# Kernel tuning notes

Hardware: AMD Instinct MI355X
Metric: run time of the kernel (lower is better)

The kernel has to match this reference:

```python
import jax, jax.numpy as jnp
import numpy as np
from jax import lax

B, S, W = 128, 256, 20
WV, CV = 50000, 100
WE, CE, CC, HID = 300, 50, 100, 512
T = 12
START, STOP, PAD = 9, 10, 11
NEG = -10000.0
H = HID // 2           # per-direction hidden
DIN = WE + CC          # LSTM input dim


def setup_inputs() -> dict:
    key = jax.random.key(0)
    ks = jax.random.split(key, 20)
    word_idxs = jax.random.randint(ks[0], (B, S), 0, WV)
    char_idxs = jax.random.randint(ks[1], (B, S, W), 0, CV)
    lengths = jax.random.randint(ks[2], (B,), S // 2, S + 1)
    mask = (jnp.arange(S)[None, :] < lengths[:, None]).astype(jnp.int32)  # prefix valid mask
    word_table = jax.random.normal(ks[3], (WV, WE), jnp.float32)
    char_table = jax.random.normal(ks[4], (CV, CE), jnp.float32)
    conv_w = jax.random.normal(ks[5], (CC, CE, 3), jnp.float32) / np.sqrt(CE * 3)
    conv_b = jnp.zeros((CC,), jnp.float32)
    sc = 1.0 / np.sqrt(H)
    u = lambda k, shp: jax.random.uniform(k, shp, jnp.float32, -sc, sc)
    w_ih_f = u(ks[6], (4 * H, DIN)); w_hh_f = u(ks[7], (4 * H, H))
    b_ih_f = u(ks[8], (4 * H,));    b_hh_f = u(ks[9], (4 * H,))
    w_ih_b = u(ks[10], (4 * H, DIN)); w_hh_b = u(ks[11], (4 * H, H))
    b_ih_b = u(ks[12], (4 * H,));   b_hh_b = u(ks[13], (4 * H,))
    h2t_w = u(ks[14], (T, HID)); h2t_b = u(ks[15], (T,))
    transitions = jax.random.normal(ks[16], (T, T), jnp.float32)
    transitions = transitions.at[START, :].set(NEG).at[:, STOP].set(NEG)
    transitions = transitions.at[PAD, :].set(NEG).at[:, PAD].set(NEG)
    return dict(word_idxs=word_idxs, char_idxs=char_idxs, mask=mask,
                word_table=word_table, char_table=char_table,
                conv_w=conv_w, conv_b=conv_b,
                w_ih_f=w_ih_f, w_hh_f=w_hh_f, b_ih_f=b_ih_f, b_hh_f=b_hh_f,
                w_ih_b=w_ih_b, w_hh_b=w_hh_b, b_ih_b=b_ih_b, b_hh_b=b_hh_b,
                h2t_w=h2t_w, h2t_b=h2t_b, transitions=transitions)


def _lstm_dir(xs, w_ih, w_hh, b, reverse):
    # xs: (S, B, DIN); torch gate order i, f, g, o
    def step(carry, x_t):
        h, c = carry
        g = x_t @ w_ih.T + h @ w_hh.T + b
        i, f, gg, o = jnp.split(g, 4, axis=-1)
        c = jax.nn.sigmoid(f) * c + jax.nn.sigmoid(i) * jnp.tanh(gg)
        h = jax.nn.sigmoid(o) * jnp.tanh(c)
        return (h, c), h
    z = jnp.zeros((xs.shape[1], w_hh.shape[1]), xs.dtype)
    _, hs = lax.scan(step, (z, z), xs, reverse=reverse)
    return hs  # (S, B, H)


def _features(word_idxs, char_idxs, word_table, char_table, conv_w, conv_b,
              w_ih_f, w_hh_f, b_ih_f, b_hh_f, w_ih_b, w_hh_b, b_ih_b, b_hh_b,
              h2t_w, h2t_b):
    we = word_table[word_idxs]                       # (B,S,WE)
    ce = char_table[char_idxs]                       # (B,S,W,CE)
    x = ce.reshape(B * S, W, CE).transpose(0, 2, 1)  # (BS,CE,W)
    conv = lax.conv_general_dilated(x, conv_w, (1,), [(1, 1)],
                                    dimension_numbers=('NCH', 'OIH', 'NCH'))
    conv = jax.nn.relu(conv + conv_b[None, :, None])
    cfeat = conv.max(axis=2).reshape(B, S, CC)       # char max-pool
    emb = jnp.concatenate([we, cfeat], axis=-1)      # (B,S,DIN)
    xs = emb.transpose(1, 0, 2)                      # (S,B,DIN)
    h_f = _lstm_dir(xs, w_ih_f, w_hh_f, b_ih_f + b_hh_f, False)
    h_b = _lstm_dir(xs, w_ih_b, w_hh_b, b_ih_b + b_hh_b, True)
    lstm_out = jnp.concatenate([h_f, h_b], axis=-1).transpose(1, 0, 2)  # (B,S,HID)
    return lstm_out @ h2t_w.T + h2t_b                # (B,S,T)


def reference(word_idxs, char_idxs, mask, word_table, char_table, conv_w, conv_b,
              w_ih_f, w_hh_f, b_ih_f, b_hh_f, w_ih_b, w_hh_b, b_ih_b, b_hh_b,
              h2t_w, h2t_b, transitions):
    feats = _features(word_idxs, char_idxs, word_table, char_table, conv_w, conv_b,
                      w_ih_f, w_hh_f, b_ih_f, b_hh_f, w_ih_b, w_hh_b, b_ih_b, b_hh_b,
                      h2t_w, h2t_b)
    # ---- batched Viterbi ----
    alpha0 = jnp.full((B, T), NEG, feats.dtype).at[:, START].set(0.0)
    def vstep(alpha, inp):
        feat_i, valid = inp                                   # (B,T), (B,)
        scores = alpha[:, :, None] + transitions[None] + feat_i[:, None, :]  # (B,prev,next)
        bp = jnp.argmax(scores, axis=1)                       # (B,T)
        new_alpha = scores.max(axis=1)
        alpha = jnp.where(valid[:, None] > 0, new_alpha, alpha)
        return alpha, bp
    alpha, bps = lax.scan(vstep, alpha0, (feats.transpose(1, 0, 2), mask.T))
    alpha = alpha + transitions[STOP][None, :]
    best_scores = alpha.max(axis=1)
    best_last = jnp.argmax(alpha, axis=1)                     # (B,)
    # ---- vectorized backtrace (skips padded tail, fills PAD) ----
    lengths = mask.sum(axis=1)
    def btstep(tag, inp):
        bp_i, i = inp
        valid = i < lengths                                   # (B,)
        out = jnp.where(valid, tag, PAD)
        prev = jnp.take_along_axis(bp_i, tag[:, None], axis=1)[:, 0]
        tag = jnp.where(valid, prev, tag)
        return tag, out
    _, path = lax.scan(btstep, best_last, (bps, jnp.arange(S)), reverse=True)
    best_paths = path.T                                       # (B,S)
    return best_scores, best_paths
```

## Files before the change

### kernel.cpp

```cpp
#include <hip/hip_runtime.h>

#define BB 128
#define SS 256
#define WW 20
#define WE 300
#define CE 50
#define CC 100
#define DIN 400
#define HID 512
#define Hh 256
#define TT 12
#define START_TAG 9
#define STOP_TAG 10
#define PAD_TAG 11
#define NEGV (-10000.0f)
#define BS 32768
#define CH 32
#define NCH 8
#define CR 4096

#define FULL_NEEDED_BYTES 96731136ull

__global__ __launch_bounds__(256) void k_embedF(
    const int* __restrict__ widx, const int* __restrict__ cidx,
    const float* __restrict__ wtab, const float* __restrict__ ctab,
    const float* __restrict__ convw, const float* __restrict__ convb,
    float* __restrict__ emb)
{
    __shared__ __align__(16) float ce_sh[2][CE][24];
    __shared__ int cid_sh[2][WW];
    __shared__ int wid_sh[2];
    const int tid = threadIdx.x;
    const int pl0 = blockIdx.x * 2;

    int g[2];
    #pragma unroll
    for (int p = 0; p < 2; p++) {
        int pl = pl0 + p;
        int s = pl >> 7, b = pl & 127;
        g[p] = b * SS + s;
    }

    if (tid < 2 * WW) {
        int p = tid / WW, w = tid % WW;
        cid_sh[p][w] = cidx[g[p] * WW + w];
    }
    if (tid < 2) wid_sh[tid] = widx[g[tid]];
    for (int i = tid; i < 2 * CE * 24; i += 256) ((float*)ce_sh)[i] = 0.f;
    __syncthreads();

    for (int i = tid; i < 2 * WW * CE; i += 256) {
        int p = i / (WW * CE);
        int rem = i % (WW * CE);
        int w = rem / CE, ce = rem % CE;
        ce_sh[p][ce][w + 1] = ctab[cid_sh[p][w] * CE + ce];
    }
    for (int i = tid; i < 2 * WE; i += 256) {
        int p = i / WE, col = i % WE;
        emb[(size_t)(pl0 + p) * DIN + col] = wtab[(size_t)wid_sh[p] * WE + col];
    }
    __syncthreads();

    const int p = tid >> 7;
    const int cc = tid & 127;
    if (cc < CC) {
        float acc[WW];
        #pragma unroll
        for (int w = 0; w < WW; w++) acc[w] = 0.f;
        for (int ce = 0; ce < CE; ce++) {
            float row[24];
            #pragma unroll
            for (int q = 0; q < 6; q++) {
                float4 v = *(const float4*)&ce_sh[p][ce][q * 4];
                row[q * 4 + 0] = v.x; row[q * 4 + 1] = v.y;
                row[q * 4 + 2] = v.z; row[q * 4 + 3] = v.w;
            }
            float c0 = convw[(cc * CE + ce) * 3 + 0];
            float c1 = convw[(cc * CE + ce) * 3 + 1];
            float c2 = convw[(cc * CE + ce) * 3 + 2];
            #pragma unroll
            for (int w = 0; w < WW; w++)
                acc[w] += c0 * row[w] + c1 * row[w + 1] + c2 * row[w + 2];
        }
        float bb = convb[cc];
        float m = 0.f;
        #pragma unroll
        for (int w = 0; w < WW; w++) {
            float v = acc[w] + bb;
            v = v > 0.f ? v : 0.f;
            m = v > m ? v : m;
        }
        emb[(size_t)(pl0 + p) * DIN + WE + cc] = m;
    }
}

__global__ __launch_bounds__(256) void k_embedC(
    const int* __restrict__ widx, const int* __restrict__ cidx,
    const float* __restrict__ wtab, const float* __restrict__ ctab,
    const float* __restrict__ convw, const float* __restrict__ convb,
    float* __restrict__ embC, int c)
{
    __shared__ __align__(16) float ce_sh[2][CE][24];
    __shared__ int cid_sh[2][WW];
    __shared__ int wid_sh[2];
    const int tid = threadIdx.x;
    const int pl0 = blockIdx.x * 2;

    int part[2], lr[2], g[2];
    #pragma unroll
    for (int p = 0; p < 2; p++) {
        int pl = pl0 + p;
        part[p] = pl >> 12;
        lr[p] = pl & 4095;
        int ls = lr[p] >> 7;
        int b = lr[p] & 127;
        int s = part[p] ? (224 - 32 * c + ls) : (32 * c + ls);
        g[p] = b * SS + s;
    }

    if (tid < 2 * WW) {
        int p = tid / WW, w = tid % WW;
        cid_sh[p][w] = cidx[g[p] * WW + w];
    }
    if (tid < 2) wid_sh[tid] = widx[g[tid]];
    for (int i = tid; i < 2 * CE * 24; i += 256) ((float*)ce_sh)[i] = 0.f;
    __syncthreads();

    for (int i = tid; i < 2 * WW * CE; i += 256) {
        int p = i / (WW * CE);
        int rem = i % (WW * CE);
        int w = rem / CE, ce = rem % CE;
        ce_sh[p][ce][w + 1] = ctab[cid_sh[p][w] * CE + ce];
    }
    for (int i = tid; i < 2 * WE; i += 256) {
        int p = i / WE, col = i % WE;
        embC[(size_t)(part[p] * CR + lr[p]) * DIN + col] =
            wtab[(size_t)wid_sh[p] * WE + col];
    }
    __syncthreads();

    const int p = tid >> 7;
    const int cc = tid & 127;
    if (cc < CC) {
        float acc[WW];
        #pragma unroll
        for (int w = 0; w < WW; w++) acc[w] = 0.f;
        for (int ce = 0; ce < CE; ce++) {
            float row[24];
            #pragma unroll
            for (int q = 0; q < 6; q++) {
                float4 v = *(const float4*)&ce_sh[p][ce][q * 4];
                row[q * 4 + 0] = v.x; row[q * 4 + 1] = v.y;
                row[q * 4 + 2] = v.z; row[q * 4 + 3] = v.w;
            }
            float c0 = convw[(cc * CE + ce) * 3 + 0];
            float c1 = convw[(cc * CE + ce) * 3 + 1];
            float c2 = convw[(cc * CE + ce) * 3 + 2];
            #pragma unroll
            for (int w = 0; w < WW; w++)
                acc[w] += c0 * row[w] + c1 * row[w + 1] + c2 * row[w + 2];
        }
        float bb = convb[cc];
        float m = 0.f;
        #pragma unroll
        for (int w = 0; w < WW; w++) {
            float v = acc[w] + bb;
            v = v > 0.f ? v : 0.f;
            m = v > m ? v : m;
        }
        embC[(size_t)(part[p] * CR + lr[p]) * DIN + WE + cc] = m;
    }
}

__global__ __launch_bounds__(256) void k_projC(
    const float* __restrict__ ef, const float* __restrict__ eb,
    const float* __restrict__ wih_f, const float* __restrict__ wih_b,
    const float* __restrict__ bih_f, const float* __restrict__ bhh_f,
    const float* __restrict__ bih_b, const float* __restrict__ bhh_b,
    float* __restrict__ gatesC)
{
    __shared__ __align__(16) float As[8][132];
    __shared__ __align__(16) float Bs[8][132];
    const int tid = threadIdx.x;
    const int rt = blockIdx.x;
    const int jt = blockIdx.y;
    const int tx = tid & 15, ty = tid >> 4;
    const int lj = tid >> 1;
    const int kh = (tid & 1) * 4;

    float acc[8][8];
    #pragma unroll
    for (int i = 0; i < 8; i++)
        #pragma unroll
        for (int j = 0; j < 8; j++) acc[i][j] = 0.f;

    const int jg = jt * 128 + lj;
    const float* wsrc = (jg < 1024) ? wih_f : wih_b;
    const int jj = jg & 1023;
    const float* esrc = (jt >= 8) ? eb : ef;

    for (int k0 = 0; k0 < DIN; k0 += 8) {
        float4 av = *(const float4*)&wsrc[(size_t)jj * DIN + k0 + kh];
        float4 bv = *(const float4*)&esrc[(size_t)(rt * 128 + lj) * DIN + k0 + kh];
        __syncthreads();
        As[kh + 0][lj] = av.x; As[kh + 1][lj] = av.y; As[kh + 2][lj] = av.z; As[kh + 3][lj] = av.w;
        Bs[kh + 0][lj] = bv.x; Bs[kh + 1][lj] = bv.y; Bs[kh + 2][lj] = bv.z; Bs[kh + 3][lj] = bv.w;
        __syncthreads();
        #pragma unroll
        for (int kk = 0; kk < 8; kk++) {
            float4 a0 = *(const float4*)&As[kk][ty * 8];
            float4 a1 = *(const float4*)&As[kk][ty * 8 + 4];
            float4 b0 = *(const float4*)&Bs[kk][tx * 8];
            float4 b1 = *(const float4*)&Bs[kk][tx * 8 + 4];
            float aa[8] = {a0.x, a0.y, a0.z, a0.w, a1.x, a1.y, a1.z, a1.w};
            float bbv[8] = {b0.x, b0.y, b0.z, b0.w, b1.x, b1.y, b1.z, b1.w};
            #pragma unroll
            for (int i = 0; i < 8; i++)
                #pragma unroll
                for (int j = 0; j < 8; j++) acc[i][j] += aa[i] * bbv[j];
        }
    }

    #pragma unroll
    for (int i = 0; i < 8; i++) {
        int j = jt * 128 + ty * 8 + i;
        int dir = j >> 10;
        int jr = j & 1023;
        float bias = dir ? (bih_b[jr] + bhh_b[jr]) : (bih_f[jr] + bhh_f[jr]);
        size_t base = (size_t)j * CR + rt * 128 + tx * 8;
        float4 o0 = {acc[i][0] + bias, acc[i][1] + bias, acc[i][2] + bias, acc[i][3] + bias};
        float4 o1 = {acc[i][4] + bias, acc[i][5] + bias, acc[i][6] + bias, acc[i][7] + bias};
        *(float4*)&gatesC[base] = o0;
        *(float4*)&gatesC[base + 4] = o1;
    }
}

__global__ __launch_bounds__(256) void k_step2(
    const float* __restrict__ gatesC,
    const float* __restrict__ whh_f, const float* __restrict__ whh_b,
    float* __restrict__ hbuf, float* __restrict__ cbuf, float* __restrict__ lstmC,
    int t)
{
    __shared__ float psum[4][128];
    const int tid = threadIdx.x;
    const int b = tid & 127;
    const int kh = tid >> 7;
    const int blk = blockIdx.x;
    const int dir = blk >> 8;
    const int kg = blk & 255;
    const int tl = t & (CH - 1);
    const int lr = (dir ? (CH - 1 - tl) : tl) * BB + b;

    float q0 = 0.f, q1 = 0.f, q2 = 0.f, q3 = 0.f, c_old = 0.f;
    const int jb = dir * 1024;
    if (kh == 0) {
        q0 = gatesC[(size_t)(jb + 0 * Hh + kg) * CR + lr];
        q1 = gatesC[(size_t)(jb + 1 * Hh + kg) * CR + lr];
        q2 = gatesC[(size_t)(jb + 2 * Hh + kg) * CR + lr];
        q3 = gatesC[(size_t)(jb + 3 * Hh + kg) * CR + lr];
        if (t > 0) c_old = cbuf[(size_t)(dir * Hh + kg) * BB + b];
    }

    float g0 = 0.f, g1 = 0.f, g2 = 0.f, g3 = 0.f;
    if (t > 0) {
        const float* whh = dir ? whh_b : whh_f;
        const int koff = __builtin_amdgcn_readfirstlane(kh * 128);
        const float* w0 = whh + (size_t)(0 * Hh + kg) * Hh + koff;
        const float* w1 = whh + (size_t)(1 * Hh + kg) * Hh + koff;
        const float* w2 = whh + (size_t)(2 * Hh + kg) * Hh + koff;
        const float* w3 = whh + (size_t)(3 * Hh + kg) * Hh + koff;
        const int par = t & 1;
        const float* hsrc = hbuf + (size_t)((par * 2 + dir) * Hh + koff) * BB;
        #pragma unroll 4
        for (int kk = 0; kk < 128; kk += 4) {
            float h0 = hsrc[(kk + 0) * BB + b];
            float h1 = hsrc[(kk + 1) * BB + b];
            float h2 = hsrc[(kk + 2) * BB + b];
            float h3 = hsrc[(kk + 3) * BB + b];
            float4 wa = *(const float4*)&w0[kk];
            float4 wb = *(const float4*)&w1[kk];
            float4 wc = *(const float4*)&w2[kk];
            float4 wd = *(const float4*)&w3[kk];
            g0 += h0 * wa.x + h1 * wa.y + h2 * wa.z + h3 * wa.w;
            g1 += h0 * wb.x + h1 * wb.y + h2 * wb.z + h3 * wb.w;
            g2 += h0 * wc.x + h1 * wc.y + h2 * wc.z + h3 * wc.w;
            g3 += h0 * wd.x + h1 * wd.y + h2 * wd.z + h3 * wd.w;
        }
    }

    if (kh) {
        psum[0][b] = g0; psum[1][b] = g1; psum[2][b] = g2; psum[3][b] = g3;
    }
    __syncthreads();
    if (!kh) {
        g0 = (q0 + g0) + psum[0][b];
        g1 = (q1 + g1) + psum[1][b];
        g2 = (q2 + g2) + psum[2][b];
        g3 = (q3 + g3) + psum[3][b];

        float si = 1.f / (1.f + expf(-g0));
        float sf = 1.f / (1.f + expf(-g1));
        float tg = tanhf(g2);
        float so = 1.f / (1.f + expf(-g3));
        float c_new = sf * c_old + si * tg;
        float h_new = so * tanhf(c_new);

        cbuf[(size_t)(dir * Hh + kg) * BB + b] = c_new;
        const int parn = (t + 1) & 1;
        hbuf[(size_t)((parn * 2 + dir) * Hh + kg) * BB + b] = h_new;
        lstmC[(size_t)(dir * Hh + kg) * CR + lr] = h_new;
    }
}

__global__ __launch_bounds__(256) void k_feats_init(
    const float* __restrict__ h2b, float* __restrict__ feats)
{
    int i = blockIdx.x * 256 + threadIdx.x;
    if (i < BS * TT) feats[i] = h2b[i % TT];
}

__global__ __launch_bounds__(256) void k_feats_acc(
    const float* __restrict__ lstmC,
    const float* __restrict__ h2w, float* __restrict__ feats, int c)
{
    __shared__ float ps[TT][128];
    const int part = blockIdx.x >> 5;
    const int ls = blockIdx.x & 31;
    const int b = threadIdx.x & 127;
    const int kh = threadIdx.x >> 7;
    const int s = part ? (224 - 32 * c + ls) : (32 * c + ls);
    const int r = s * BB + b;
    const int k0 = kh * 128;

    float acc[TT];
    #pragma unroll
    for (int t = 0; t < TT; t++) acc[t] = 0.f;
    for (int dk = 0; dk < 128; dk++) {
        float v = lstmC[(size_t)(part * Hh + k0 + dk) * CR + ls * BB + b];
        #pragma unroll
        for (int t = 0; t < TT; t++) acc[t] += v * h2w[t * HID + part * Hh + k0 + dk];
    }
    if (kh) {
        #pragma unroll
        for (int t = 0; t < TT; t++) ps[t][b] = acc[t];
    }
    __syncthreads();
    if (!kh) {
        #pragma unroll
        for (int t = 0; t < TT; t++)
            feats[(size_t)r * TT + t] += acc[t] + ps[t][b];
    }
}

__global__ __launch_bounds__(64) void k_viterbi(
    const float* __restrict__ feats,
    const int* __restrict__ mask, const float* __restrict__ trans,
    float* __restrict__ out)
{
    __shared__ unsigned char bp_sh[SS][TT];
    __shared__ int red[64];
    __shared__ int len_sh;
    const int b = blockIdx.x;
    const int tid = threadIdx.x;
    const int n = tid;

    int partial = 0;
    for (int s = tid; s < SS; s += 64) partial += mask[b * SS + s];
    red[tid] = partial;
    __syncthreads();
    if (tid == 0) {
        int L = 0;
        for (int i = 0; i < 64; i++) L += red[i];
        len_sh = L;
    }
    __syncthreads();
    const int len = len_sh;

    float tr[TT];
    float alpha = NEGV;
    if (n < TT) {
        #pragma unroll
        for (int p = 0; p < TT; p++) tr[p] = trans[p * TT + n];
        alpha = (n == START_TAG) ? 0.f : NEGV;
    }

    for (int s = 0; s < len; s++) {
        float feat = (n < TT) ? feats[(size_t)(s * BB + b) * TT + n] : 0.f;
        float best = -3.0e38f;
        int bpi = 0;
        #pragma unroll
        for (int p = 0; p < TT; p++) {
            float ap = __shfl(alpha, p, 64);
            float sc = (n < TT) ? ((ap + tr[p]) + feat) : -3.0e38f;
            if (sc > best) { best = sc; bpi = p; }
        }
        if (n < TT) {
            bp_sh[s][n] = (unsigned char)bpi;
            alpha = best;
        }
    }

    float term = (n < TT) ? (alpha + trans[STOP_TAG * TT + n]) : -3.0e38f;
    float bs = -3.0e38f;
    int bl = 0;
    #pragma unroll
    for (int p = 0; p < TT; p++) {
        float v = __shfl(term, p, 64);
        if (v > bs) { bs = v; bl = p; }
    }

    if (tid == 0) {
        out[b] = bs;
        int tag = bl;
        for (int s = SS - 1; s >= 0; s--) {
            float o;
            if (s < len) {
                o = (float)tag;
                tag = (int)bp_sh[s][tag];
            } else {
                o = (float)PAD_TAG;
            }
            out[BB + b * SS + s] = o;
        }
    }
}

extern "C" void kernel_launch(void* const* d_in, const int* in_sizes, int n_in,
                              void* d_out, int out_size, void* d_ws, size_t ws_size,
                              hipStream_t stream) {
    const int*   widx  = (const int*)d_in[0];
    const int*   cidx  = (const int*)d_in[1];
    const int*   mask  = (const int*)d_in[2];
    const float* wtab  = (const float*)d_in[3];
    const float* ctab  = (const float*)d_in[4];
    const float* convw = (const float*)d_in[5];
    const float* convb = (const float*)d_in[6];
    const float* wih_f = (const float*)d_in[7];
    const float* whh_f = (const float*)d_in[8];
    const float* bih_f = (const float*)d_in[9];
    const float* bhh_f = (const float*)d_in[10];
    const float* wih_b = (const float*)d_in[11];
    const float* whh_b = (const float*)d_in[12];
    const float* bih_b = (const float*)d_in[13];
    const float* bhh_b = (const float*)d_in[14];
    const float* h2w   = (const float*)d_in[15];
    const float* h2b   = (const float*)d_in[16];
    const float* trans = (const float*)d_in[17];

    const bool full = ws_size >= FULL_NEEDED_BYTES;
    float* ws = (float*)d_ws;
    float* emb    = ws;
    const size_t emb_fl = full ? (size_t)BS * DIN : (size_t)2 * CR * DIN;
    float* gatesC = emb + emb_fl;
    float* lstmC  = gatesC + (size_t)2048 * CR;
    float* feats  = lstmC + (size_t)HID * CR;
    float* hbuf   = feats + (size_t)BS * TT;
    float* cbuf   = hbuf + (size_t)4 * Hh * BB;

    hipLaunchKernelGGL(k_feats_init, dim3((BS * TT + 255) / 256), dim3(256), 0, stream,
                       h2b, feats);
    if (full) {
        hipLaunchKernelGGL(k_embedF, dim3(BS / 2), dim3(256), 0, stream,
                           widx, cidx, wtab, ctab, convw, convb, emb);
    }
    for (int c = 0; c < NCH; c++) {
        if (!full) {
            hipLaunchKernelGGL(k_embedC, dim3(CR), dim3(256), 0, stream,
                               widx, cidx, wtab, ctab, convw, convb, emb, c);
        }
        const float* ef = full ? (emb + (size_t)(32 * c * BB) * DIN) : emb;
        const float* eb = full ? (emb + (size_t)((224 - 32 * c) * BB) * DIN)
                               : (emb + (size_t)CR * DIN);
        hipLaunchKernelGGL(k_projC, dim3(CR / 128, 16), dim3(256), 0, stream,
                           ef, eb, wih_f, wih_b, bih_f, bhh_f, bih_b, bhh_b, gatesC);
        for (int tl = 0; tl < CH; tl++) {
            hipLaunchKernelGGL(k_step2, dim3(512), dim3(256), 0, stream,
                               gatesC, whh_f, whh_b, hbuf, cbuf, lstmC, c * CH + tl);
        }
        hipLaunchKernelGGL(k_feats_acc, dim3(64), dim3(256), 0, stream,
                           lstmC, h2w, feats, c);
    }
    hipLaunchKernelGGL(k_viterbi, dim3(BB), dim3(64), 0, stream, feats, mask, trans, (float*)d_out);
}
```

Measured before the change: 3.417 ms.

## Restructure LSTM recurrent step into per-thread full-K dot products with batch-major hidden state

The recurrent step kernel now gives each thread one (batch, hidden-unit) pair and loops over the whole 256-wide hidden input, instead of splitting K across two half-blocks joined by a shared-memory reduction. The hidden-state buffer is switched to batch-major so each thread can read its row with float4 loads. The grid is halved to 256 blocks, and the syncthreads and idle half-block in the epilogue are gone. The cost is a serial loop twice as long per thread, strided rather than coalesced h loads across lanes, and weight loads that are no longer wave-uniform.

```diff
diff --git a/kernel.cpp b/kernel.cpp
--- a/kernel.cpp
+++ b/kernel.cpp
@@ -235,81 +235,64 @@
     }
 }
 
-__global__ __launch_bounds__(256) void k_step2(
+__global__ __launch_bounds__(256) void k_step3(
     const float* __restrict__ gatesC,
     const float* __restrict__ whh_f, const float* __restrict__ whh_b,
     float* __restrict__ hbuf, float* __restrict__ cbuf, float* __restrict__ lstmC,
     int t)
 {
-    __shared__ float psum[4][128];
     const int tid = threadIdx.x;
-    const int b = tid & 127;
-    const int kh = tid >> 7;
+    const int bb = tid & 31;
+    const int ko = tid >> 5;
     const int blk = blockIdx.x;
-    const int dir = blk >> 8;
-    const int kg = blk & 255;
+    const int dir = blk >> 7;
+    const int kot = (blk >> 2) & 31;
+    const int bq  = blk & 3;
+    const int b   = bq * 32 + bb;
+    const int kout = kot * 8 + ko;
     const int tl = t & (CH - 1);
-    const int lr = (dir ? (CH - 1 - tl) : tl) * BB + b;
-
-    float q0 = 0.f, q1 = 0.f, q2 = 0.f, q3 = 0.f, c_old = 0.f;
-    const int jb = dir * 1024;
-    if (kh == 0) {
-        q0 = gatesC[(size_t)(jb + 0 * Hh + kg) * CR + lr];
-        q1 = gatesC[(size_t)(jb + 1 * Hh + kg) * CR + lr];
-        q2 = gatesC[(size_t)(jb + 2 * Hh + kg) * CR + lr];
-        q3 = gatesC[(size_t)(jb + 3 * Hh + kg) * CR + lr];
-        if (t > 0) c_old = cbuf[(size_t)(dir * Hh + kg) * BB + b];
-    }
-
-    float g0 = 0.f, g1 = 0.f, g2 = 0.f, g3 = 0.f;
+    const int ls = dir ? (CH - 1 - tl) : tl;
+    const int lr = ls * BB + b;
+    const int jb = dir * 4 * Hh;
+
+    float g0 = gatesC[(size_t)(jb + 0 * Hh + kout) * CR + lr];
+    float g1 = gatesC[(size_t)(jb + 1 * Hh + kout) * CR + lr];
+    float g2 = gatesC[(size_t)(jb + 2 * Hh + kout) * CR + lr];
+    float g3 = gatesC[(size_t)(jb + 3 * Hh + kout) * CR + lr];
+    float c_old = 0.f;
+    if (t > 0) c_old = cbuf[(dir * Hh + kout) * BB + b];
+
     if (t > 0) {
         const float* whh = dir ? whh_b : whh_f;
-        const int koff = __builtin_amdgcn_readfirstlane(kh * 128);
-        const float* w0 = whh + (size_t)(0 * Hh + kg) * Hh + koff;
-        const float* w1 = whh + (size_t)(1 * Hh + kg) * Hh + koff;
-        const float* w2 = whh + (size_t)(2 * Hh + kg) * Hh + koff;
-        const float* w3 = whh + (size_t)(3 * Hh + kg) * Hh + koff;
-        const int par = t & 1;
-        const float* hsrc = hbuf + (size_t)((par * 2 + dir) * Hh + koff) * BB;
+        const float* w0 = whh + (size_t)(0 * Hh + kout) * Hh;
+        const float* w1 = whh + (size_t)(1 * Hh + kout) * Hh;
+        const float* w2 = whh + (size_t)(2 * Hh + kout) * Hh;
+        const float* w3 = whh + (size_t)(3 * Hh + kout) * Hh;
+        const float* hrow = hbuf + (size_t)(((t & 1) * 2 + dir) * BB + b) * Hh;
         #pragma unroll 4
-        for (int kk = 0; kk < 128; kk += 4) {
-            float h0 = hsrc[(kk + 0) * BB + b];
-            float h1 = hsrc[(kk + 1) * BB + b];
-            float h2 = hsrc[(kk + 2) * BB + b];
-            float h3 = hsrc[(kk + 3) * BB + b];
-            float4 wa = *(const float4*)&w0[kk];
-            float4 wb = *(const float4*)&w1[kk];
-            float4 wc = *(const float4*)&w2[kk];
-            float4 wd = *(const float4*)&w3[kk];
-            g0 += h0 * wa.x + h1 * wa.y + h2 * wa.z + h3 * wa.w;
-            g1 += h0 * wb.x + h1 * wb.y + h2 * wb.z + h3 * wb.w;
-            g2 += h0 * wc.x + h1 * wc.y + h2 * wc.z + h3 * wc.w;
-            g3 += h0 * wd.x + h1 * wd.y + h2 * wd.z + h3 * wd.w;
-        }
-    }
-
-    if (kh) {
-        psum[0][b] = g0; psum[1][b] = g1; psum[2][b] = g2; psum[3][b] = g3;
-    }
-    __syncthreads();
-    if (!kh) {
-        g0 = (q0 + g0) + psum[0][b];
-        g1 = (q1 + g1) + psum[1][b];
-        g2 = (q2 + g2) + psum[2][b];
-        g3 = (q3 + g3) + psum[3][b];
-
-        float si = 1.f / (1.f + expf(-g0));
-        float sf = 1.f / (1.f + expf(-g1));
-        float tg = tanhf(g2);
-        float so = 1.f / (1.f + expf(-g3));
-        float c_new = sf * c_old + si * tg;
-        float h_new = so * tanhf(c_new);
-
-        cbuf[(size_t)(dir * Hh + kg) * BB + b] = c_new;
-        const int parn = (t + 1) & 1;
-        hbuf[(size_t)((parn * 2 + dir) * Hh + kg) * BB + b] = h_new;
-        lstmC[(size_t)(dir * Hh + kg) * CR + lr] = h_new;
-    }
+        for (int kin = 0; kin < Hh; kin += 4) {
+            float4 hv = *(const float4*)&hrow[kin];
+            float4 wa = *(const float4*)&w0[kin];
+            float4 wb = *(const float4*)&w1[kin];
+            float4 wc = *(const float4*)&w2[kin];
+            float4 wd = *(const float4*)&w3[kin];
+            g0 += hv.x * wa.x + hv.y * wa.y + hv.z * wa.z + hv.w * wa.w;
+            g1 += hv.x * wb.x + hv.y * wb.y + hv.z * wb.z + hv.w * wb.w;
+            g2 += hv.x * wc.x + hv.y * wc.y + hv.z * wc.z + hv.w * wc.w;
+            g3 += hv.x * wd.x + hv.y * wd.y + hv.z * wd.z + hv.w * wd.w;
+        }
+    }
+
+    float si = 1.f / (1.f + expf(-g0));
+    float sf = 1.f / (1.f + expf(-g1));
+    float tg = tanhf(g2);
+    float so = 1.f / (1.f + expf(-g3));
+    float c_new = sf * c_old + si * tg;
+    float h_new = so * tanhf(c_new);
+
+    cbuf[(dir * Hh + kout) * BB + b] = c_new;
+    hbuf[(size_t)((((t + 1) & 1) * 2 + dir) * BB + b) * Hh + kout] = h_new;
+    lstmC[(size_t)(dir * Hh + kout) * CR + lr] = h_new;
 }
 
 __global__ __launch_bounds__(256) void k_feats_init(
@@ -474,7 +457,7 @@
         hipLaunchKernelGGL(k_projC, dim3(CR / 128, 16), dim3(256), 0, stream,
                            ef, eb, wih_f, wih_b, bih_f, bhh_f, bih_b, bhh_b, gatesC);
         for (int tl = 0; tl < CH; tl++) {
-            hipLaunchKernelGGL(k_step2, dim3(512), dim3(256), 0, stream,
+            hipLaunchKernelGGL(k_step3, dim3(256), dim3(256), 0, stream,
                                gatesC, whh_f, whh_b, hbuf, cbuf, lstmC, c * CH + tl);
         }
         hipLaunchKernelGGL(k_feats_acc, dim3(64), dim3(256), 0, stream,
```

Measured after the change: 6.610 ms. +93.4%, slower.

## Use bf16 MFMA for LSTM input projection with bf16 embeddings and weights

Applied to the files above, without the earlier changes.

Replaces the fp32 SIMT GEMM for the per-chunk input projection with a bf16 MFMA (16x16x32) kernel. Embeddings are now written as bf16 with K padded to 416, and a new pre-pass converts W_ih to bf16 and precomputes the fused biases. The aim is to cut the compute and bandwidth cost of the projection GEMM, at the price of bf16 rounding on the inputs, which could affect accuracy. The workspace layout is reorganized around byte-size constants.

```diff
diff --git a/kernel.cpp b/kernel.cpp
--- a/kernel.cpp
+++ b/kernel.cpp
@@ -7,6 +7,7 @@
 #define CE 50
 #define CC 100
 #define DIN 400
+#define KP 416
 #define HID 512
 #define Hh 256
 #define TT 12
@@ -19,13 +20,51 @@
 #define NCH 8
 #define CR 4096
 
-#define FULL_NEEDED_BYTES 96731136ull
+typedef __attribute__((ext_vector_type(8))) short short8;
+typedef __attribute__((ext_vector_type(4))) float floatx4;
+
+#define SZ_EMB_FULL  27262976ull
+#define SZ_EMB_CHUNK  6815744ull
+#define SZ_WB         1703936ull
+#define SZ_BIAS          8192ull
+#define SZ_GATES     33554432ull
+#define SZ_LSTM       8388608ull
+#define SZ_FEATS      1572864ull
+#define SZ_HBUF        524288ull
+#define SZ_CBUF        262144ull
+#define FULL_NEEDED_BYTES (SZ_EMB_FULL + SZ_WB + SZ_BIAS + SZ_GATES + SZ_LSTM + SZ_FEATS + SZ_HBUF + SZ_CBUF)
+
+__device__ __forceinline__ unsigned short f2bf(float x) {
+    unsigned int u = __builtin_bit_cast(unsigned int, x);
+    unsigned int r = (u + 0x7FFFu + ((u >> 16) & 1u)) >> 16;
+    return (unsigned short)r;
+}
+
+__global__ __launch_bounds__(256) void k_w2b(
+    const float* __restrict__ wih_f, const float* __restrict__ wih_b,
+    const float* __restrict__ bih_f, const float* __restrict__ bhh_f,
+    const float* __restrict__ bih_b, const float* __restrict__ bhh_b,
+    unsigned short* __restrict__ wB, float* __restrict__ biasC)
+{
+    int idx = blockIdx.x * 256 + threadIdx.x;
+    if (idx < 2048 * KP) {
+        int j = idx / KP;
+        int col = idx - j * KP;
+        const float* src = (j < 1024) ? wih_f : wih_b;
+        int jr = j & 1023;
+        wB[idx] = (col < DIN) ? f2bf(src[jr * DIN + col]) : 0;
+    }
+    if (idx < 2048) {
+        int jr = idx & 1023;
+        biasC[idx] = (idx < 1024) ? (bih_f[jr] + bhh_f[jr]) : (bih_b[jr] + bhh_b[jr]);
+    }
+}
 
 __global__ __launch_bounds__(256) void k_embedF(
     const int* __restrict__ widx, const int* __restrict__ cidx,
     const float* __restrict__ wtab, const float* __restrict__ ctab,
     const float* __restrict__ convw, const float* __restrict__ convb,
-    float* __restrict__ emb)
+    unsigned short* __restrict__ embB)
 {
     __shared__ __align__(16) float ce_sh[2][CE][24];
     __shared__ int cid_sh[2][WW];
@@ -57,7 +96,11 @@
     }
     for (int i = tid; i < 2 * WE; i += 256) {
         int p = i / WE, col = i % WE;
-        emb[(size_t)(pl0 + p) * DIN + col] = wtab[(size_t)wid_sh[p] * WE + col];
+        embB[(size_t)(pl0 + p) * KP + col] = f2bf(wtab[(size_t)wid_sh[p] * WE + col]);
+    }
+    for (int i = tid; i < 2 * (KP - DIN); i += 256) {
+        int p = i / (KP - DIN), col = DIN + i % (KP - DIN);
+        embB[(size_t)(pl0 + p) * KP + col] = 0;
     }
     __syncthreads();
 
@@ -90,7 +133,7 @@
             v = v > 0.f ? v : 0.f;
             m = v > m ? v : m;
         }
-        emb[(size_t)(pl0 + p) * DIN + WE + cc] = m;
+        embB[(size_t)(pl0 + p) * KP + WE + cc] = f2bf(m);
     }
 }
 
@@ -98,7 +141,7 @@
     const int* __restrict__ widx, const int* __restrict__ cidx,
     const float* __restrict__ wtab, const float* __restrict__ ctab,
     const float* __restrict__ convw, const float* __restrict__ convb,
-    float* __restrict__ embC, int c)
+    unsigned short* __restrict__ embB, int c)
 {
     __shared__ __align__(16) float ce_sh[2][CE][24];
     __shared__ int cid_sh[2][WW];
@@ -134,8 +177,12 @@
     }
     for (int i = tid; i < 2 * WE; i += 256) {
         int p = i / WE, col = i % WE;
-        embC[(size_t)(part[p] * CR + lr[p]) * DIN + col] =
-            wtab[(size_t)wid_sh[p] * WE + col];
+        embB[(size_t)(part[p] * CR + lr[p]) * KP + col] =
+            f2bf(wtab[(size_t)wid_sh[p] * WE + col]);
+    }
+    for (int i = tid; i < 2 * (KP - DIN); i += 256) {
+        int p = i / (KP - DIN), col = DIN + i % (KP - DIN);
+        embB[(size_t)(part[p] * CR + lr[p]) * KP + col] = 0;
     }
     __syncthreads();
 
@@ -168,70 +215,82 @@
             v = v > 0.f ? v : 0.f;
             m = v > m ? v : m;
         }
-        embC[(size_t)(part[p] * CR + lr[p]) * DIN + WE + cc] = m;
-    }
-}
-
-__global__ __launch_bounds__(256) void k_projC(
-    const float* __restrict__ ef, const float* __restrict__ eb,
-    const float* __restrict__ wih_f, const float* __restrict__ wih_b,
-    const float* __restrict__ bih_f, const float* __restrict__ bhh_f,
-    const float* __restrict__ bih_b, const float* __restrict__ bhh_b,
+        embB[(size_t)(part[p] * CR + lr[p]) * KP + WE + cc] = f2bf(m);
+    }
+}
+
+__global__ __launch_bounds__(256) void k_projB(
+    const unsigned short* __restrict__ ef, const unsigned short* __restrict__ eb,
+    const unsigned short* __restrict__ wB, const float* __restrict__ biasC,
     float* __restrict__ gatesC)
 {
-    __shared__ __align__(16) float As[8][132];
-    __shared__ __align__(16) float Bs[8][132];
+    __shared__ __align__(16) unsigned short Wt[128 * 40];
+    __shared__ __align__(16) unsigned short Et[128 * 40];
     const int tid = threadIdx.x;
     const int rt = blockIdx.x;
     const int jt = blockIdx.y;
-    const int tx = tid & 15, ty = tid >> 4;
-    const int lj = tid >> 1;
-    const int kh = (tid & 1) * 4;
-
-    float acc[8][8];
-    #pragma unroll
-    for (int i = 0; i < 8; i++)
-        #pragma unroll
-        for (int j = 0; j < 8; j++) acc[i][j] = 0.f;
-
-    const int jg = jt * 128 + lj;
-    const float* wsrc = (jg < 1024) ? wih_f : wih_b;
-    const int jj = jg & 1023;
-    const float* esrc = (jt >= 8) ? eb : ef;
-
-    for (int k0 = 0; k0 < DIN; k0 += 8) {
-        float4 av = *(const float4*)&wsrc[(size_t)jj * DIN + k0 + kh];
-        float4 bv = *(const float4*)&esrc[(size_t)(rt * 128 + lj) * DIN + k0 + kh];
+    const unsigned short* esrc = (jt >= 8) ? eb : ef;
+
+    const int row = tid >> 1;
+    const int half = tid & 1;
+    const int lane = tid & 63;
+    const int wv = tid >> 6;
+    const int wm = wv >> 1, wn = wv & 1;
+    const int fr = lane & 15, quad = lane >> 4;
+
+    floatx4 acc[4][4];
+    #pragma unroll
+    for (int i = 0; i < 4; i++)
+        #pragma unroll
+        for (int j = 0; j < 4; j++) acc[i][j] = (floatx4){0.f, 0.f, 0.f, 0.f};
+
+    const unsigned short* wrow = wB + (size_t)(jt * 128 + row) * KP + half * 16;
+    const unsigned short* erow = esrc + (size_t)(rt * 128 + row) * KP + half * 16;
+
+    for (int kt = 0; kt < 13; kt++) {
+        int4 wv0 = *(const int4*)(wrow + kt * 32);
+        int4 wv1 = *(const int4*)(wrow + kt * 32 + 8);
+        int4 ev0 = *(const int4*)(erow + kt * 32);
+        int4 ev1 = *(const int4*)(erow + kt * 32 + 8);
         __syncthreads();
-        As[kh + 0][lj] = av.x; As[kh + 1][lj] = av.y; As[kh + 2][lj] = av.z; As[kh + 3][lj] = av.w;
-        Bs[kh + 0][lj] = bv.x; Bs[kh + 1][lj] = bv.y; Bs[kh + 2][lj] = bv.z; Bs[kh + 3][lj] = bv.w;
+        *(int4*)&Wt[row * 40 + half * 16]     = wv0;
+        *(int4*)&Wt[row * 40 + half * 16 + 8] = wv1;
+        *(int4*)&Et[row * 40 + half * 16]     = ev0;
+        *(int4*)&Et[row * 40 + half * 16 + 8] = ev1;
         __syncthreads();
-        #pragma unroll
-        for (int kk = 0; kk < 8; kk++) {
-            float4 a0 = *(const float4*)&As[kk][ty * 8];
-            float4 a1 = *(const float4*)&As[kk][ty * 8 + 4];
-            float4 b0 = *(const float4*)&Bs[kk][tx * 8];
-            float4 b1 = *(const float4*)&Bs[kk][tx * 8 + 4];
-            float aa[8] = {a0.x, a0.y, a0.z, a0.w, a1.x, a1.y, a1.z, a1.w};
-            float bbv[8] = {b0.x, b0.y, b0.z, b0.w, b1.x, b1.y, b1.z, b1.w};
+
+        short8 af[4], bf[4];
+        #pragma unroll
+        for (int fi = 0; fi < 4; fi++)
+            af[fi] = *(const short8*)&Wt[(wm * 64 + fi * 16 + fr) * 40 + quad * 8];
+        #pragma unroll
+        for (int fj = 0; fj < 4; fj++)
+            bf[fj] = *(const short8*)&Et[(wn * 64 + fj * 16 + fr) * 40 + quad * 8];
+        #pragma unroll
+        for (int fi = 0; fi < 4; fi++)
             #pragma unroll
-            for (int i = 0; i < 8; i++)
-                #pragma unroll
-                for (int j = 0; j < 8; j++) acc[i][j] += aa[i] * bbv[j];
-        }
-    }
-
-    #pragma unroll
-    for (int i = 0; i < 8; i++) {
-        int j = jt * 128 + ty * 8 + i;
-        int dir = j >> 10;
-        int jr = j & 1023;
-        float bias = dir ? (bih_b[jr] + bhh_b[jr]) : (bih_f[jr] + bhh_f[jr]);
-        size_t base = (size_t)j * CR + rt * 128 + tx * 8;
-        float4 o0 = {acc[i][0] + bias, acc[i][1] + bias, acc[i][2] + bias, acc[i][3] + bias};
-        float4 o1 = {acc[i][4] + bias, acc[i][5] + bias, acc[i][6] + bias, acc[i][7] + bias};
-        *(float4*)&gatesC[base] = o0;
-        *(float4*)&gatesC[base + 4] = o1;
+            for (int fj = 0; fj < 4; fj++)
+                acc[fi][fj] = __builtin_amdgcn_mfma_f32_16x16x32_bf16(
+                    af[fi], bf[fj], acc[fi][fj], 0, 0, 0);
+    }
+
+    float bias[4][4];
+    #pragma unroll
+    for (int fi = 0; fi < 4; fi++)
+        #pragma unroll
+        for (int reg = 0; reg < 4; reg++)
+            bias[fi][reg] = biasC[jt * 128 + wm * 64 + fi * 16 + quad * 4 + reg];
+
+    #pragma unroll
+    for (int fi = 0; fi < 4; fi++) {
+        #pragma unroll
+        for (int fj = 0; fj < 4; fj++) {
+            int rg = rt * 128 + wn * 64 + fj * 16 + fr;
+            int jg = jt * 128 + wm * 64 + fi * 16 + quad * 4;
+            #pragma unroll
+            for (int reg = 0; reg < 4; reg++)
+                gatesC[(size_t)(jg + reg) * CR + rg] = acc[fi][fj][reg] + bias[fi][reg];
+        }
     }
 }
 
@@ -448,31 +507,35 @@
     const float* trans = (const float*)d_in[17];
 
     const bool full = ws_size >= FULL_NEEDED_BYTES;
-    float* ws = (float*)d_ws;
-    float* emb    = ws;
-    const size_t emb_fl = full ? (size_t)BS * DIN : (size_t)2 * CR * DIN;
-    float* gatesC = emb + emb_fl;
-    float* lstmC  = gatesC + (size_t)2048 * CR;
-    float* feats  = lstmC + (size_t)HID * CR;
-    float* hbuf   = feats + (size_t)BS * TT;
-    float* cbuf   = hbuf + (size_t)4 * Hh * BB;
+    char* base = (char*)d_ws;
+    const size_t emb_sz = full ? SZ_EMB_FULL : SZ_EMB_CHUNK;
+    unsigned short* embB = (unsigned short*)base;
+    unsigned short* wB   = (unsigned short*)(base + emb_sz);
+    float* biasC  = (float*)(base + emb_sz + SZ_WB);
+    float* gatesC = (float*)(base + emb_sz + SZ_WB + SZ_BIAS);
+    float* lstmC  = (float*)(base + emb_sz + SZ_WB + SZ_BIAS + SZ_GATES);
+    float* feats  = (float*)(base + emb_sz + SZ_WB + SZ_BIAS + SZ_GATES + SZ_LSTM);
+    float* hbuf   = (float*)(base + emb_sz + SZ_WB + SZ_BIAS + SZ_GATES + SZ_LSTM + SZ_FEATS);
+    float* cbuf   = (float*)(base + emb_sz + SZ_WB + SZ_BIAS + SZ_GATES + SZ_LSTM + SZ_FEATS + SZ_HBUF);
 
     hipLaunchKernelGGL(k_feats_init, dim3((BS * TT + 255) / 256), dim3(256), 0, stream,
                        h2b, feats);
+    hipLaunchKernelGGL(k_w2b, dim3((2048 * KP + 255) / 256), dim3(256), 0, stream,
+                       wih_f, wih_b, bih_f, bhh_f, bih_b, bhh_b, wB, biasC);
     if (full) {
         hipLaunchKernelGGL(k_embedF, dim3(BS / 2), dim3(256), 0, stream,
-                           widx, cidx, wtab, ctab, convw, convb, emb);
+                           widx, cidx, wtab, ctab, convw, convb, embB);
     }
     for (int c = 0; c < NCH; c++) {
         if (!full) {
             hipLaunchKernelGGL(k_embedC, dim3(CR), dim3(256), 0, stream,
-                               widx, cidx, wtab, ctab, convw, convb, emb, c);
-        }
-        const float* ef = full ? (emb + (size_t)(32 * c * BB) * DIN) : emb;
-        const float* eb = full ? (emb + (size_t)((224 - 32 * c) * BB) * DIN)
-                               : (emb + (size_t)CR * DIN);
-        hipLaunchKernelGGL(k_projC, dim3(CR / 128, 16), dim3(256), 0, stream,
-                           ef, eb, wih_f, wih_b, bih_f, bhh_f, bih_b, bhh_b, gatesC);
+                               widx, cidx, wtab, ctab, convw, convb, embB, c);
+        }
+        const unsigned short* ef = full ? (embB + (size_t)(32 * c * BB) * KP) : embB;
+        const unsigned short* eb = full ? (embB + (size_t)((224 - 32 * c) * BB) * KP)
+                                        : (embB + (size_t)CR * KP);
+        hipLaunchKernelGGL(k_projB, dim3(32, 16), dim3(256), 0, stream,
+                           ef, eb, wB, biasC, gatesC);
         for (int tl = 0; tl < CH; tl++) {
             hipLaunchKernelGGL(k_step2, dim3(512), dim3(256), 0, stream,
                                gatesC, whh_f, whh_b, hbuf, cbuf, lstmC, c * CH + tl);
```

Result: faster. 2.859 ms (-16.3%).
